# Kernel tuning notes

Hardware: AMD Instinct MI355X
Metric: run time of the kernel (lower is better)

## Reference

```python
import jax, jax.numpy as jnp
import numpy as np


def _maxpool2x2(x):
    # x: [B, H, W, C] -> [B, H//2, W//2, C], VALID 2x2/2 max pool
    B, H, W, C = x.shape
    return x.reshape(B, H // 2, 2, W // 2, 2, C).max(axis=(2, 4))


def setup_inputs() -> dict:
    key = jax.random.key(0)
    ks = jax.random.split(key, 6)
    B, H, W, C = 16, 64, 64, 512
    x = jax.random.normal(ks[0], (B, H, W, C), dtype=jnp.float32)
    w_theta = jax.random.normal(ks[1], (C, C // 8), dtype=jnp.float32) * 0.02
    w_phi = jax.random.normal(ks[2], (C, C // 8), dtype=jnp.float32) * 0.02
    w_g = jax.random.normal(ks[3], (C, C // 2), dtype=jnp.float32) * 0.02
    w_o = jax.random.normal(ks[4], (C // 2, C), dtype=jnp.float32) * 0.02
    return {
        "x": x,
        "w_theta": w_theta, "b_theta": jnp.zeros((C // 8,), jnp.float32),
        "w_phi": w_phi, "b_phi": jnp.zeros((C // 8,), jnp.float32),
        "w_g": w_g, "b_g": jnp.zeros((C // 2,), jnp.float32),
        "w_o": w_o, "b_o": jnp.zeros((C,), jnp.float32),
        "sigma": jnp.ones((1,), jnp.float32) * 0.1,
    }


def reference(x, w_theta, b_theta, w_phi, b_phi, w_g, b_g, w_o, b_o, sigma):
    B, H, W, C = x.shape
    n_feat = H * W
    # 1x1 convs are channel-mixing GEMMs over pixels
    theta = (jnp.einsum('bhwc,cd->bhwd', x, w_theta) + b_theta).reshape(B, n_feat, C // 8)
    phi = _maxpool2x2(jnp.einsum('bhwc,cd->bhwd', x, w_phi) + b_phi).reshape(B, n_feat // 4, C // 8)
    g = _maxpool2x2(jnp.einsum('bhwc,cd->bhwd', x, w_g) + b_g).reshape(B, n_feat // 4, C // 2)
    # [B, HW, HW/4] attention (no scaling, matching SAGAN/tf source)
    attn = jax.nn.softmax(jnp.einsum('bqd,bkd->bqk', theta, phi), axis=-1)
    attn_g = jnp.einsum('bqk,bkd->bqd', attn, g).reshape(B, H, W, C // 2)
    attn_g = jnp.einsum('bhwd,dc->bhwc', attn_g, w_o) + b_o
    return x + sigma * attn_g
```

## Files before the change

kernel.cpp:

```cpp
#include <hip/hip_runtime.h>
#include <math.h>

#define NB    16
#define NPIX  4096
#define NPOOL 1024
#define CIN   512
#define CD    64
#define CG    256

typedef unsigned short u16;
typedef unsigned int   u32;
typedef __attribute__((ext_vector_type(8)))  u16    u16x8;
typedef __attribute__((ext_vector_type(8)))  __bf16 bf16x8;
typedef __attribute__((ext_vector_type(16))) float  f32x16;

__device__ __forceinline__ u16 f2bf(float x) {
    u32 u = __builtin_bit_cast(u32, x);
    u += 0x7fffu + ((u >> 16) & 1u);
    return (u16)(u >> 16);
}
__device__ __forceinline__ float bf2f(u16 h) {
    u32 u = ((u32)h) << 16;
    return __builtin_bit_cast(float, u);
}
__device__ __forceinline__ f32x16 mfma32(u16x8 a, u16x8 b, f32x16 c) {
    return __builtin_amdgcn_mfma_f32_32x32x16_bf16(
        __builtin_bit_cast(bf16x8, a), __builtin_bit_cast(bf16x8, b), c, 0, 0, 0);
}

__global__ __launch_bounds__(256) void prep_kernel(
    const float* __restrict__ wt, const float* __restrict__ wp,
    const float* __restrict__ wg, const float* __restrict__ wo,
    const float* __restrict__ bt, const float* __restrict__ bp,
    const float* __restrict__ bg,
    u16* __restrict__ WT, u16* __restrict__ WOT, float* __restrict__ biasP)
{
    const int bx = blockIdx.x;
    const int t  = threadIdx.x;

    if (bx == 320) {
        for (int i = t; i < 384; i += 256)
            biasP[i] = (i < 64) ? bt[i] : (i < 128) ? bp[i - 64] : bg[i - 128];
        return;
    }

    const float* src; u16* dst; int N, K, kt, nt;
    if (bx < 32)       { src = wt; dst = WT;             N = 64;  K = 512; kt = bx >> 1;        nt = bx & 1; }
    else if (bx < 64)  { src = wp; dst = WT + 64 * 512;  N = 64;  K = 512; kt = (bx - 32) >> 1; nt = (bx - 32) & 1; }
    else if (bx < 192) { src = wg; dst = WT + 128 * 512; N = 256; K = 512; kt = (bx - 64) >> 3; nt = (bx - 64) & 7; }
    else               { src = wo; dst = WOT;            N = 512; K = 256; kt = (bx - 192) >> 4; nt = (bx - 192) & 15; }

    __shared__ float tile[32][33];
    {
        int r  = t >> 3;
        int c4 = (t & 7) * 4;
        float4 v = *(const float4*)(src + (size_t)(kt * 32 + r) * N + nt * 32 + c4);
        tile[r][c4]     = v.x;
        tile[r][c4 + 1] = v.y;
        tile[r][c4 + 2] = v.z;
        tile[r][c4 + 3] = v.w;
    }
    __syncthreads();
    {
        int n  = t >> 3;
        int k4 = (t & 7) * 4;
        ushort4 wv;
        wv.x = f2bf(tile[k4][n]);
        wv.y = f2bf(tile[k4 + 1][n]);
        wv.z = f2bf(tile[k4 + 2][n]);
        wv.w = f2bf(tile[k4 + 3][n]);
        *(ushort4*)(dst + (size_t)(nt * 32 + n) * K + kt * 32 + k4) = wv;
    }
}

#define AST 40
__global__ __launch_bounds__(256) void proj_gemm_kernel(
    const float* __restrict__ x, const u16* __restrict__ WT,
    const float* __restrict__ biasP,
    u16* __restrict__ theta, u16* __restrict__ phiF, u16* __restrict__ gF)
{
    __shared__ u16 As[128 * AST];
    __shared__ u16 Bs[128 * AST];

    const int t  = threadIdx.x;
    const int w  = t >> 6, l = t & 63, lr = l & 31, lh = l >> 5;
    const int sb = (blockIdx.x & 7) * 192 + (blockIdx.x >> 3);
    const int mt = sb / 3, nt = sb % 3;
    const int m0 = mt * 128, n0 = nt * 128;
    const int mw = (w & 1) * 64, nw = (w >> 1) * 64;

    const int srow = t >> 1;
    const int sks  = (t & 1) * 16;

    f32x16 acc[2][2] = {};

    for (int k0 = 0; k0 < 512; k0 += 32) {
        {
            const float4* ap = (const float4*)(x + (size_t)(m0 + srow) * 512 + k0 + sks);
            float4 v0 = ap[0], v1 = ap[1], v2 = ap[2], v3 = ap[3];
            u16x8 a0, a1;
            a0[0] = f2bf(v0.x); a0[1] = f2bf(v0.y); a0[2] = f2bf(v0.z); a0[3] = f2bf(v0.w);
            a0[4] = f2bf(v1.x); a0[5] = f2bf(v1.y); a0[6] = f2bf(v1.z); a0[7] = f2bf(v1.w);
            a1[0] = f2bf(v2.x); a1[1] = f2bf(v2.y); a1[2] = f2bf(v2.z); a1[3] = f2bf(v2.w);
            a1[4] = f2bf(v3.x); a1[5] = f2bf(v3.y); a1[6] = f2bf(v3.z); a1[7] = f2bf(v3.w);
            *(u16x8*)&As[srow * AST + sks]     = a0;
            *(u16x8*)&As[srow * AST + sks + 8] = a1;
        }
        {
            const u16x8* bp = (const u16x8*)(WT + (size_t)(n0 + srow) * 512 + k0 + sks);
            *(u16x8*)&Bs[srow * AST + sks]     = bp[0];
            *(u16x8*)&Bs[srow * AST + sks + 8] = bp[1];
        }
        __syncthreads();
#pragma unroll
        for (int ki = 0; ki < 2; ++ki) {
            u16x8 af0 = *(const u16x8*)&As[(mw + lr)      * AST + ki * 16 + lh * 8];
            u16x8 af1 = *(const u16x8*)&As[(mw + 32 + lr) * AST + ki * 16 + lh * 8];
            u16x8 bf0 = *(const u16x8*)&Bs[(nw + lr)      * AST + ki * 16 + lh * 8];
            u16x8 bf1 = *(const u16x8*)&Bs[(nw + 32 + lr) * AST + ki * 16 + lh * 8];
            acc[0][0] = mfma32(af0, bf0, acc[0][0]);
            acc[0][1] = mfma32(af0, bf1, acc[0][1]);
            acc[1][0] = mfma32(af1, bf0, acc[1][0]);
            acc[1][1] = mfma32(af1, bf1, acc[1][1]);
        }
        __syncthreads();
    }

#pragma unroll
    for (int mi = 0; mi < 2; ++mi) {
#pragma unroll
        for (int ni = 0; ni < 2; ++ni) {
            const int nb = n0 + nw + ni * 32;
            const int n  = nb + lr;
            const float bv = biasP[n];
            u16* dst; int ld, col;
            if (nb < 64)        { dst = theta; ld = 64;  col = n; }
            else if (nb < 128)  { dst = phiF;  ld = 64;  col = n - 64; }
            else                { dst = gF;    ld = 256; col = n - 128; }
#pragma unroll
            for (int r = 0; r < 16; ++r) {
                int row = m0 + mw + mi * 32 + (r & 3) + 8 * (r >> 2) + 4 * lh;
                dst[(size_t)row * ld + col] = f2bf(acc[mi][ni][r] + bv);
            }
        }
    }
}

__global__ __launch_bounds__(256) void pool_kernel(
    const u16* __restrict__ phiF, const u16* __restrict__ gF,
    u16* __restrict__ phi, u16* __restrict__ gt)
{
    const int t  = threadIdx.x;
    const int b  = blockIdx.x >> 5;
    const int ph = blockIdx.x & 31;

    {
        const int pw = t >> 3, dq = (t & 7) * 8;
        const u16* base = phiF + ((size_t)(b * NPIX + 2 * ph * 64 + 2 * pw)) * 64 + dq;
        u16x8 v00 = *(const u16x8*)(base);
        u16x8 v01 = *(const u16x8*)(base + 64);
        u16x8 v10 = *(const u16x8*)(base + 64 * 64);
        u16x8 v11 = *(const u16x8*)(base + 64 * 64 + 64);
        u16x8 m;
#pragma unroll
        for (int j = 0; j < 8; ++j) {
            float mf = fmaxf(fmaxf(bf2f(v00[j]), bf2f(v01[j])),
                             fmaxf(bf2f(v10[j]), bf2f(v11[j])));
            m[j] = f2bf(mf);
        }
        *(u16x8*)(phi + ((size_t)(b * NPOOL + ph * 32 + pw)) * 64 + dq) = m;
    }
    {
        const u16* gb = gF + ((size_t)(b * NPIX + 2 * ph * 64)) * 256 + t;
        u16 buf[32];
#pragma unroll
        for (int kp = 0; kp < 32; ++kp) {
            float m = fmaxf(
                fmaxf(bf2f(gb[(size_t)(2 * kp) * 256]),      bf2f(gb[(size_t)(2 * kp + 1) * 256])),
                fmaxf(bf2f(gb[(size_t)(64 + 2 * kp) * 256]), bf2f(gb[(size_t)(64 + 2 * kp + 1) * 256])));
            buf[kp] = f2bf(m);
        }
        u16* go = gt + ((size_t)(b * CG + t)) * NPOOL + ph * 32;
#pragma unroll
        for (int j = 0; j < 4; ++j)
            *(u16x8*)(go + j * 8) = *(const u16x8*)&buf[j * 8];
    }
}

#define SLD 1032
__global__ __launch_bounds__(512) void attn_mfma_kernel(
    const u16* __restrict__ theta, const u16* __restrict__ phi,
    const u16* __restrict__ gt, u16* __restrict__ attn_g)
{
    __shared__ u16   S[32 * SLD];
    __shared__ float rinv[32];

    const int t  = threadIdx.x;
    const int w  = t >> 6;
    const int l  = t & 63;
    const int lr = l & 31;
    const int lh = l >> 5;
    const int sb = (blockIdx.x & 7) * 256 + (blockIdx.x >> 3);
    const int b  = sb >> 7;
    const int q0 = (sb & 127) * 32;

    const u16* thb = theta + ((size_t)(b * NPIX + q0 + lr)) * CD + lh * 8;
    u16x8 afr[4];
#pragma unroll
    for (int ki = 0; ki < 4; ++ki)
        afr[ki] = *(const u16x8*)(thb + ki * 16);

    const u16* phb = phi + (size_t)b * NPOOL * CD;
#pragma unroll 2
    for (int nt = 0; nt < 4; ++nt) {
        int k0 = w * 128 + nt * 32;
        const u16* pb = phb + (size_t)(k0 + lr) * CD + lh * 8;
        f32x16 acc = {};
#pragma unroll
        for (int ki = 0; ki < 4; ++ki)
            acc = mfma32(afr[ki], *(const u16x8*)(pb + ki * 16), acc);
#pragma unroll
        for (int r = 0; r < 16; ++r) {
            int row = (r & 3) + 8 * (r >> 2) + 4 * lh;
            S[row * SLD + k0 + lr] = f2bf(acc[r]);
        }
    }
    __syncthreads();

    {
        const int row = t >> 4, cg = t & 15;
        u16* srow = S + row * SLD;
        float mx = -1e30f;
#pragma unroll
        for (int i = 0; i < 8; ++i) {
            u16x8 v = *(const u16x8*)(srow + cg * 8 + 128 * i);
#pragma unroll
            for (int j = 0; j < 8; ++j) mx = fmaxf(mx, bf2f(v[j]));
        }
        mx = fmaxf(mx, __shfl_xor(mx, 1));
        mx = fmaxf(mx, __shfl_xor(mx, 2));
        mx = fmaxf(mx, __shfl_xor(mx, 4));
        mx = fmaxf(mx, __shfl_xor(mx, 8));
        float sum = 0.f;
#pragma unroll
        for (int i = 0; i < 8; ++i) {
            u16* p = srow + cg * 8 + 128 * i;
            u16x8 v = *(const u16x8*)p;
            u16x8 e;
#pragma unroll
            for (int j = 0; j < 8; ++j) {
                float ev = __expf(bf2f(v[j]) - mx);
                sum += ev;
                e[j] = f2bf(ev);
            }
            *(u16x8*)p = e;
        }
        sum += __shfl_xor(sum, 1);
        sum += __shfl_xor(sum, 2);
        sum += __shfl_xor(sum, 4);
        sum += __shfl_xor(sum, 8);
        if (cg == 0) rinv[row] = 1.0f / sum;
    }
    __syncthreads();

    const u16* gtb  = gt + (size_t)b * CG * NPOOL;
    const u16* gp   = gtb + (size_t)(w * 32 + lr) * NPOOL + lh * 8;
    const u16* arow = S + lr * SLD + lh * 8;
    f32x16 oa = {}, ob2 = {};
#pragma unroll 4
    for (int k0 = 0; k0 < NPOOL; k0 += 32) {
        u16x8 a0 = *(const u16x8*)(arow + k0);
        u16x8 a1 = *(const u16x8*)(arow + k0 + 16);
        u16x8 b0 = *(const u16x8*)(gp + k0);
        u16x8 b1 = *(const u16x8*)(gp + k0 + 16);
        oa  = mfma32(a0, b0, oa);
        ob2 = mfma32(a1, b1, ob2);
    }

    u16* obp = attn_g + ((size_t)(b * NPIX + q0)) * CG;
#pragma unroll
    for (int r = 0; r < 16; ++r) {
        int qrow = (r & 3) + 8 * (r >> 2) + 4 * lh;
        float inv = rinv[qrow];
        obp[(size_t)qrow * CG + w * 32 + lr] = f2bf((oa[r] + ob2[r]) * inv);
    }
}

__global__ __launch_bounds__(256) void out_gemm_kernel(
    const u16* __restrict__ attn_gB, const u16* __restrict__ WOT,
    const float* __restrict__ x, const float* __restrict__ bo,
    const float* __restrict__ sigma, float* __restrict__ out)
{
    __shared__ u16 As[128 * AST];
    __shared__ u16 Bs[128 * AST];

    const int t  = threadIdx.x;
    const int w  = t >> 6, l = t & 63, lr = l & 31, lh = l >> 5;
    const int sb = (blockIdx.x & 7) * 256 + (blockIdx.x >> 3);
    const int mt = sb >> 2, nt = sb & 3;
    const int m0 = mt * 128, n0 = nt * 128;
    const int mw = (w & 1) * 64, nw = (w >> 1) * 64;

    const int srow = t >> 1;
    const int sks  = (t & 1) * 16;

    f32x16 acc[2][2] = {};

    for (int k0 = 0; k0 < 256; k0 += 32) {
        {
            const u16x8* ap = (const u16x8*)(attn_gB + (size_t)(m0 + srow) * 256 + k0 + sks);
            *(u16x8*)&As[srow * AST + sks]     = ap[0];
            *(u16x8*)&As[srow * AST + sks + 8] = ap[1];
        }
        {
            const u16x8* bp = (const u16x8*)(WOT + (size_t)(n0 + srow) * 256 + k0 + sks);
            *(u16x8*)&Bs[srow * AST + sks]     = bp[0];
            *(u16x8*)&Bs[srow * AST + sks + 8] = bp[1];
        }
        __syncthreads();
#pragma unroll
        for (int ki = 0; ki < 2; ++ki) {
            u16x8 af0 = *(const u16x8*)&As[(mw + lr)      * AST + ki * 16 + lh * 8];
            u16x8 af1 = *(const u16x8*)&As[(mw + 32 + lr) * AST + ki * 16 + lh * 8];
            u16x8 bf0 = *(const u16x8*)&Bs[(nw + lr)      * AST + ki * 16 + lh * 8];
            u16x8 bf1 = *(const u16x8*)&Bs[(nw + 32 + lr) * AST + ki * 16 + lh * 8];
            acc[0][0] = mfma32(af0, bf0, acc[0][0]);
            acc[0][1] = mfma32(af0, bf1, acc[0][1]);
            acc[1][0] = mfma32(af1, bf0, acc[1][0]);
            acc[1][1] = mfma32(af1, bf1, acc[1][1]);
        }
        __syncthreads();
    }

    const float s = sigma[0];
#pragma unroll
    for (int mi = 0; mi < 2; ++mi) {
#pragma unroll
        for (int ni = 0; ni < 2; ++ni) {
            const int n  = n0 + nw + ni * 32 + lr;
            const float bv = bo[n];
#pragma unroll
            for (int r = 0; r < 16; ++r) {
                int row = m0 + mw + mi * 32 + (r & 3) + 8 * (r >> 2) + 4 * lh;
                size_t idx = (size_t)row * 512 + n;
                out[idx] = x[idx] + s * (acc[mi][ni][r] + bv);
            }
        }
    }
}

extern "C" void kernel_launch(void* const* d_in, const int* in_sizes, int n_in,
                              void* d_out, int out_size, void* d_ws, size_t ws_size,
                              hipStream_t stream)
{
    const float* x     = (const float*)d_in[0];
    const float* wt    = (const float*)d_in[1];
    const float* bt    = (const float*)d_in[2];
    const float* wp    = (const float*)d_in[3];
    const float* bp    = (const float*)d_in[4];
    const float* wg    = (const float*)d_in[5];
    const float* bg    = (const float*)d_in[6];
    const float* wo    = (const float*)d_in[7];
    const float* bo    = (const float*)d_in[8];
    const float* sigma = (const float*)d_in[9];
    float* out = (float*)d_out;

    char* ws = (char*)d_ws;
    u16*   theta   = (u16*)(ws);
    u16*   phi     = (u16*)(ws + ((size_t)8  << 20));
    u16*   phiF    = (u16*)(ws + ((size_t)10 << 20));
    u16*   gF      = (u16*)(ws + ((size_t)18 << 20));
    u16*   attn_gB = (u16*)(ws + ((size_t)10 << 20));
    u16*   gt      = (u16*)(ws + ((size_t)50 << 20));
    u16*   WT      = (u16*)(ws + ((size_t)58 << 20));
    u16*   WOT     = (u16*)(ws + ((size_t)58 << 20) + (384 << 10));
    float* biasP   = (float*)(ws + ((size_t)58 << 20) + (640 << 10));

    prep_kernel<<<321, 256, 0, stream>>>(wt, wp, wg, wo, bt, bp, bg, WT, WOT, biasP);
    proj_gemm_kernel<<<512 * 3, 256, 0, stream>>>(x, WT, biasP, theta, phiF, gF);
    pool_kernel<<<NB * 32, 256, 0, stream>>>(phiF, gF, phi, gt);
    attn_mfma_kernel<<<NB * NPIX / 32, 512, 0, stream>>>(theta, phi, gt, attn_gB);
    out_gemm_kernel<<<512 * 4, 256, 0, stream>>>(attn_gB, WOT, x, bo, sigma, out);
}
```

Measured before the change: 494.6 us.

## Process 64 query rows per attention block to reuse phi and g loads

The attention kernel now handles 64 query rows per block instead of 32, so each phi fragment and each g fragment loaded from global memory feeds two MFMA row tiles. This halves global traffic for phi and gt per query and halves the grid size. In exchange the block uses about twice the shared memory (64 rows of S, roughly 132 KB) and more accumulator registers, which may lower occupancy to one block per CU and reduce latency hiding.

Result: faster. 450.4 us (-8.9%).

```diff
diff --git a/kernel.cpp b/kernel.cpp
--- a/kernel.cpp
+++ b/kernel.cpp
@@ -192,59 +192,67 @@
     const u16* __restrict__ theta, const u16* __restrict__ phi,
     const u16* __restrict__ gt, u16* __restrict__ attn_g)
 {
-    __shared__ u16   S[32 * SLD];
-    __shared__ float rinv[32];
+    __shared__ u16   S[64 * SLD];
+    __shared__ float rinv[64];
 
     const int t  = threadIdx.x;
     const int w  = t >> 6;
     const int l  = t & 63;
     const int lr = l & 31;
     const int lh = l >> 5;
-    const int sb = (blockIdx.x & 7) * 256 + (blockIdx.x >> 3);
-    const int b  = sb >> 7;
-    const int q0 = (sb & 127) * 32;
-
-    const u16* thb = theta + ((size_t)(b * NPIX + q0 + lr)) * CD + lh * 8;
-    u16x8 afr[4];
-#pragma unroll
-    for (int ki = 0; ki < 4; ++ki)
-        afr[ki] = *(const u16x8*)(thb + ki * 16);
+    const int sb = (blockIdx.x & 7) * 128 + (blockIdx.x >> 3);
+    const int b  = sb >> 6;
+    const int q0 = (sb & 63) * 64;
+
+    const u16* thb0 = theta + ((size_t)(b * NPIX + q0 + lr)) * CD + lh * 8;
+    const u16* thb1 = thb0 + (size_t)32 * CD;
+    u16x8 af0[4], af1[4];
+#pragma unroll
+    for (int ki = 0; ki < 4; ++ki) {
+        af0[ki] = *(const u16x8*)(thb0 + ki * 16);
+        af1[ki] = *(const u16x8*)(thb1 + ki * 16);
+    }
 
     const u16* phb = phi + (size_t)b * NPOOL * CD;
 #pragma unroll 2
     for (int nt = 0; nt < 4; ++nt) {
         int k0 = w * 128 + nt * 32;
         const u16* pb = phb + (size_t)(k0 + lr) * CD + lh * 8;
-        f32x16 acc = {};
-#pragma unroll
-        for (int ki = 0; ki < 4; ++ki)
-            acc = mfma32(afr[ki], *(const u16x8*)(pb + ki * 16), acc);
+        u16x8 pf0 = *(const u16x8*)(pb);
+        u16x8 pf1 = *(const u16x8*)(pb + 16);
+        u16x8 pf2 = *(const u16x8*)(pb + 32);
+        u16x8 pf3 = *(const u16x8*)(pb + 48);
+        f32x16 acc0 = {}, acc1 = {};
+        acc0 = mfma32(af0[0], pf0, acc0);  acc1 = mfma32(af1[0], pf0, acc1);
+        acc0 = mfma32(af0[1], pf1, acc0);  acc1 = mfma32(af1[1], pf1, acc1);
+        acc0 = mfma32(af0[2], pf2, acc0);  acc1 = mfma32(af1[2], pf2, acc1);
+        acc0 = mfma32(af0[3], pf3, acc0);  acc1 = mfma32(af1[3], pf3, acc1);
 #pragma unroll
         for (int r = 0; r < 16; ++r) {
             int row = (r & 3) + 8 * (r >> 2) + 4 * lh;
-            S[row * SLD + k0 + lr] = f2bf(acc[r]);
+            S[row * SLD + k0 + lr]        = f2bf(acc0[r]);
+            S[(32 + row) * SLD + k0 + lr] = f2bf(acc1[r]);
         }
     }
     __syncthreads();
 
     {
-        const int row = t >> 4, cg = t & 15;
+        const int row = t >> 3, cg = t & 7;
         u16* srow = S + row * SLD;
         float mx = -1e30f;
 #pragma unroll
-        for (int i = 0; i < 8; ++i) {
-            u16x8 v = *(const u16x8*)(srow + cg * 8 + 128 * i);
+        for (int i = 0; i < 16; ++i) {
+            u16x8 v = *(const u16x8*)(srow + cg * 8 + 64 * i);
 #pragma unroll
             for (int j = 0; j < 8; ++j) mx = fmaxf(mx, bf2f(v[j]));
         }
         mx = fmaxf(mx, __shfl_xor(mx, 1));
         mx = fmaxf(mx, __shfl_xor(mx, 2));
         mx = fmaxf(mx, __shfl_xor(mx, 4));
-        mx = fmaxf(mx, __shfl_xor(mx, 8));
         float sum = 0.f;
 #pragma unroll
-        for (int i = 0; i < 8; ++i) {
-            u16* p = srow + cg * 8 + 128 * i;
+        for (int i = 0; i < 16; ++i) {
+            u16* p = srow + cg * 8 + 64 * i;
             u16x8 v = *(const u16x8*)p;
             u16x8 e;
 #pragma unroll
@@ -258,31 +266,36 @@
         sum += __shfl_xor(sum, 1);
         sum += __shfl_xor(sum, 2);
         sum += __shfl_xor(sum, 4);
-        sum += __shfl_xor(sum, 8);
         if (cg == 0) rinv[row] = 1.0f / sum;
     }
     __syncthreads();
 
-    const u16* gtb  = gt + (size_t)b * CG * NPOOL;
-    const u16* gp   = gtb + (size_t)(w * 32 + lr) * NPOOL + lh * 8;
-    const u16* arow = S + lr * SLD + lh * 8;
-    f32x16 oa = {}, ob2 = {};
+    const u16* gp  = gt + ((size_t)(b * CG + w * 32 + lr)) * NPOOL + lh * 8;
+    const u16* ar0 = S + lr * SLD + lh * 8;
+    const u16* ar1 = S + (32 + lr) * SLD + lh * 8;
+    f32x16 o0a = {}, o0b = {}, o1a = {}, o1b = {};
 #pragma unroll 4
     for (int k0 = 0; k0 < NPOOL; k0 += 32) {
-        u16x8 a0 = *(const u16x8*)(arow + k0);
-        u16x8 a1 = *(const u16x8*)(arow + k0 + 16);
-        u16x8 b0 = *(const u16x8*)(gp + k0);
-        u16x8 b1 = *(const u16x8*)(gp + k0 + 16);
-        oa  = mfma32(a0, b0, oa);
-        ob2 = mfma32(a1, b1, ob2);
+        u16x8 b0  = *(const u16x8*)(gp + k0);
+        u16x8 b1  = *(const u16x8*)(gp + k0 + 16);
+        u16x8 a00 = *(const u16x8*)(ar0 + k0);
+        u16x8 a01 = *(const u16x8*)(ar0 + k0 + 16);
+        u16x8 a10 = *(const u16x8*)(ar1 + k0);
+        u16x8 a11 = *(const u16x8*)(ar1 + k0 + 16);
+        o0a = mfma32(a00, b0, o0a);
+        o0b = mfma32(a01, b1, o0b);
+        o1a = mfma32(a10, b0, o1a);
+        o1b = mfma32(a11, b1, o1b);
     }
 
     u16* obp = attn_g + ((size_t)(b * NPIX + q0)) * CG;
 #pragma unroll
     for (int r = 0; r < 16; ++r) {
         int qrow = (r & 3) + 8 * (r >> 2) + 4 * lh;
-        float inv = rinv[qrow];
-        obp[(size_t)qrow * CG + w * 32 + lr] = f2bf((oa[r] + ob2[r]) * inv);
+        float inv0 = rinv[qrow];
+        float inv1 = rinv[32 + qrow];
+        obp[(size_t)qrow * CG + w * 32 + lr]        = f2bf((o0a[r] + o0b[r]) * inv0);
+        obp[(size_t)(32 + qrow) * CG + w * 32 + lr] = f2bf((o1a[r] + o1b[r]) * inv1);
     }
 }
 
@@ -379,6 +392,6 @@
     prep_kernel<<<321, 256, 0, stream>>>(wt, wp, wg, wo, bt, bp, bg, WT, WOT, biasP);
     proj_gemm_kernel<<<512 * 3, 256, 0, stream>>>(x, WT, biasP, theta, phiF, gF);
     pool_kernel<<<NB * 32, 256, 0, stream>>>(phiF, gF, phi, gt);
-    attn_mfma_kernel<<<NB * NPIX / 32, 512, 0, stream>>>(theta, phi, gt, attn_gB);
+    attn_mfma_kernel<<<NB * NPIX / 64, 512, 0, stream>>>(theta, phi, gt, attn_gB);
     out_gemm_kernel<<<512 * 4, 256, 0, stream>>>(attn_gB, WOT, x, bo, sigma, out);
 }
```
